# Kernel tuning notes

Measured on AMD Instinct MI355X. Metric: run time of the kernel, lower is better.

The kernel has to match this reference:

```python
import jax, jax.numpy as jnp
import numpy as np

KS = 5          # kernel_size
D = 2           # spatial dim
DX = 0.01       # region kernel spacing
SCALE = 1.0
NX, NY = 32, 32
N = NX * NY


def _region_kernel():
    # gaussians.region_kernel: KS x KS grid of offsets spaced DX, centered at 0
    off = (jnp.arange(KS, dtype=jnp.float32) - (KS - 1) / 2.0) * DX
    gx, gy = jnp.meshgrid(off, off, indexing='ij')
    return jnp.stack([gx, gy], -1).reshape(-1, D)  # (KS*KS, 2)


def _build_cov(scaling, transform):
    # Cholesky-style parameterization: L lower-triangular with diag=scaling,
    # off-diag=transform; cov = L @ L^T (d=2 closed form)
    s0, s1 = scaling[:, 0], scaling[:, 1]
    t = transform[:, 0]
    c00 = s0 * s0
    c01 = s0 * t
    c11 = t * t + s1 * s1
    return jnp.stack([jnp.stack([c00, c01], -1), jnp.stack([c01, c11], -1)], -2)


def _inv2x2(c):
    det = c[:, 0, 0] * c[:, 1, 1] - c[:, 0, 1] * c[:, 1, 0]
    inv = jnp.stack([jnp.stack([c[:, 1, 1], -c[:, 0, 1]], -1),
                     jnp.stack([-c[:, 1, 0], c[:, 0, 0]], -1)], -2)
    return inv / det[:, None, None]


def setup_inputs() -> dict:
    key = jax.random.key(0)
    ks = jax.random.split(key, 20)
    # Gaussian state: grid means as in __init__
    tx = jnp.linspace(-1.0, 1.0, NX) * SCALE
    ty = jnp.linspace(-1.0, 1.0, NY) * SCALE
    gx, gy = jnp.meshgrid(tx, ty, indexing='ij')
    means = jnp.stack([gx, gy], -1).reshape(-1, D).astype(jnp.float32)
    u = 0.1 * jax.random.normal(ks[0], (N, 1), jnp.float32)
    scaling = jnp.exp(-4.5 + 0.2 * jax.random.normal(ks[1], (N, D), jnp.float32)) * SCALE
    transform = 0.002 * jax.random.normal(ks[2], (N, 1), jnp.float32)
    opacities = 2.0 + 0.1 * jax.random.normal(ks[3], (N,), jnp.float32)
    # network weights (4 heads share the first 3 layer shapes)
    convW = 0.05 * jax.random.normal(ks[4], (4, 50, 3, KS, KS), jnp.float32)
    convb = 0.01 * jax.random.normal(ks[5], (4, 50), jnp.float32)
    embW = 0.3 * jax.random.normal(ks[6], (4, 7, 30), jnp.float32)
    embb = 0.01 * jax.random.normal(ks[7], (4, 30), jnp.float32)
    l1W = 0.1 * jax.random.normal(ks[8], (4, 80, 80), jnp.float32)
    l1b = 0.01 * jax.random.normal(ks[9], (4, 80), jnp.float32)
    outW_sol = 0.1 * jax.random.normal(ks[10], (80, 1), jnp.float32)
    outb_sol = 0.01 * jax.random.normal(ks[11], (1,), jnp.float32)
    outW_trans = 0.1 * jax.random.normal(ks[12], (80, 2), jnp.float32)
    outb_trans = 0.01 * jax.random.normal(ks[13], (2,), jnp.float32)
    outW_scale = 0.1 * jax.random.normal(ks[14], (80, 2), jnp.float32)
    outb_scale = 0.01 * jax.random.normal(ks[15], (2,), jnp.float32)
    outW_tform = 0.1 * jax.random.normal(ks[16], (80, 1), jnp.float32)
    outb_tform = 0.01 * jax.random.normal(ks[17], (1,), jnp.float32)
    return {"means": means, "u": u, "scaling": scaling, "transform": transform,
            "opacities": opacities, "convW": convW, "convb": convb,
            "embW": embW, "embb": embb, "l1W": l1W, "l1b": l1b,
            "outW_sol": outW_sol, "outb_sol": outb_sol,
            "outW_trans": outW_trans, "outb_trans": outb_trans,
            "outW_scale": outW_scale, "outb_scale": outb_scale,
            "outW_tform": outW_tform, "outb_tform": outb_tform}


def reference(means, u, scaling, transform, opacities, convW, convb, embW, embb,
              l1W, l1b, outW_sol, outb_sol, outW_trans, outb_trans,
              outW_scale, outb_scale, outW_tform, outb_tform):
    n = means.shape[0]
    cov = _build_cov(scaling, transform)          # (N,2,2)
    conics = _inv2x2(cov)                         # (N,2,2)

    # --- sampling (torch.no_grad block in original) ---
    kern = _region_kernel()                                        # (25,2)
    samples = (means[:, None, :] + kern[None]).reshape(-1, D)      # (M,2), M=N*25
    bc = jnp.all(jnp.abs(samples) < SCALE, -1).astype(means.dtype)[:, None]
    alpha = jax.nn.sigmoid(opacities)                              # (N,)
    diff = samples[:, None, :] - means[None, :, :]                 # (M,N,2)
    Cq = jnp.einsum('nij,mnj->mni', conics, diff)                  # (M,N,2)
    G = jnp.exp(-0.5 * jnp.einsum('mni,mni->mn', diff, Cq)) * alpha[None, :]  # (M,N)
    u_s = G @ u                                                    # (M,1)
    # DIFFUSION pde_rhs = trace of laplacian: sum_n G * (|C q|^2 - tr(C)) * u_n
    trC = conics[:, 0, 0] + conics[:, 1, 1]
    lap = jnp.einsum('mn,mn,nc->mc', G, (Cq ** 2).sum(-1) - trC[None, :], u)  # (M,1)
    in_samples = jax.lax.stop_gradient(jnp.concatenate([u_s, lap, bc], -1))   # (M,3)

    # (N, 25, 3) -> (N, 3, 5, 5)
    img = in_samples.reshape(n, KS * KS, -1).transpose(0, 2, 1).reshape(n, -1, KS, KS)
    in_params = jnp.concatenate([means, u, scaling, transform, opacities[:, None]], -1)  # (N,7)

    # 4 Networks: conv(5x5 -> 1x1, 50ch) + param embed(7->30) + MLP(80->80->out)
    y = jnp.tanh(jnp.einsum('ncij,kocij->kno', img, convW) + convb[:, None, :])   # (4,N,50)
    e = jnp.tanh(jnp.einsum('nf,kfg->kng', in_params, embW) + embb[:, None, :])   # (4,N,30)
    h = jnp.tanh(jnp.einsum('knf,kfg->kng', jnp.concatenate([y, e], -1), l1W)
                 + l1b[:, None, :])                                               # (4,N,80)

    deltas = h[0] @ outW_sol + outb_sol          # (N,1)
    translation = h[1] @ outW_trans + outb_trans # (N,2)
    dscale = h[2] @ outW_scale + outb_scale      # (N,2)
    dtransform = h[3] @ outW_tform + outb_tform  # (N,1)

    u_new = u + deltas
    means_new = means + translation
    scaling_new = scaling * jnp.exp(dscale)
    transform_new = transform + dtransform
    cov_new = _build_cov(scaling_new, transform_new)
    return (u_new, means_new, scaling_new, transform_new, cov_new)
```

## Files before the change

kernel.cpp:

```cpp
#include <hip/hip_runtime.h>
#include <hip/hip_bf16.h>


#define NG 1024

__device__ __forceinline__ float tanh_fast(float x) {
    return 1.0f - 2.0f / (__expf(2.0f * x) + 1.0f);
}

__global__ __launch_bounds__(256) void k_fused(
    const float* __restrict__ means, const float* __restrict__ u,
    const float* __restrict__ scal, const float* __restrict__ trans,
    const float* __restrict__ opac,
    const float* __restrict__ convW, const float* __restrict__ convb,
    const float* __restrict__ embW,  const float* __restrict__ embb,
    const float* __restrict__ l1W,   const float* __restrict__ l1b,
    const float* __restrict__ oWs,  const float* __restrict__ obs,
    const float* __restrict__ oWt,  const float* __restrict__ obt,
    const float* __restrict__ oWsc, const float* __restrict__ obsc,
    const float* __restrict__ oWtf, const float* __restrict__ obtf,
    float* __restrict__ out)
{
    __shared__ float gcomp[NG * 8];
    __shared__ float pus[2][2][32];
    __shared__ float plap[2][2][32];
    __shared__ float simg[2][80];
    __shared__ float hin[2][4][80];
    __shared__ float hv[2][4][80];
    __shared__ float semb[840];
    __shared__ float sembb[120];
    __shared__ float shead[480];
    __shared__ float sheadb[6];
    __shared__ int   cnt;

    const int t  = threadIdx.x;
    const int n0 = blockIdx.x * 2;

    const float mx0 = means[2*n0],   my0 = means[2*n0+1];
    const float mx1 = means[2*n0+2], my1 = means[2*n0+3];
    const float uu0 = u[n0],     uu1 = u[n0+1];
    const float sc00 = scal[2*n0],   sc01 = scal[2*n0+1];
    const float sc10 = scal[2*n0+2], sc11 = scal[2*n0+3];
    const float tr0 = trans[n0], tr1 = trans[n0+1];
    const float op0 = opac[n0],  op1 = opac[n0+1];

    float wcv[75];
    {
        const float* w = convW + (size_t)(t < 200 ? t : 0) * 75;
        #pragma unroll
        for (int j = 0; j < 75; ++j) wcv[j] = w[j];
    }
    float w1[80];
    {
        int k = t / 80, g = t - (t / 80) * 80;
        const float* w = l1W + (size_t)(k * 80) * 80 + g;
        #pragma unroll
        for (int f = 0; f < 80; ++f) w1[f] = w[f * 80];
    }
    float bcv  = (t < 200) ? convb[t] : 0.0f;
    float b1   = l1b[t];
    float b1k3 = l1b[256 + (t & 63)];

    for (int i = t; i < 840; i += 256) semb[i] = embW[i];
    if (t < 120) sembb[t] = embb[t];
    for (int i = t; i < 480; i += 256) {
        float v = (i < 80) ? oWs[i] : (i < 240) ? oWt[i - 80]
                : (i < 400) ? oWsc[i - 240] : oWtf[i - 400];
        shead[i] = v;
    }
    if (t < 6) sheadb[t] = (t == 0) ? obs[0] : (t < 3) ? obt[t-1]
                         : (t < 5) ? obsc[t-3] : obtf[0];

    const float bxmin = fminf(mx0, mx1) - 0.02f, bxmax = fmaxf(mx0, mx1) + 0.02f;
    const float bymin = fminf(my0, my1) - 0.02f, bymax = fmaxf(my0, my1) + 0.02f;

    if (t == 0) cnt = 0;
    __syncthreads();
    for (int g = t; g < NG; g += 256) {
        float gmx = means[2*g], gmy = means[2*g+1];
        float s0  = scal[2*g],  s1  = scal[2*g+1];
        float tt  = trans[g];
        float c00 = s0*s0, c01 = s0*tt, c11 = tt*tt + s1*s1;
        float r2  = 100.0f * (c00 + c11);
        float ddx = fmaxf(fmaxf(bxmin - gmx, gmx - bxmax), 0.0f);
        float ddy = fmaxf(fmaxf(bymin - gmy, gmy - bymax), 0.0f);
        if (ddx*ddx + ddy*ddy <= r2) {
            float idet = 1.0f / (c00*c11 - c01*c01);
            float A = c11*idet, B = -c01*idet, C = c00*idet;
            float alpha = 1.0f / (1.0f + __expf(-opac[g]));
            int slot = atomicAdd(&cnt, 1);
            float4* dst = (float4*)(gcomp + slot*8);
            dst[0] = make_float4(gmx, gmy, A, B);
            dst[1] = make_float4(C, A + C, alpha * u[g], 0.0f);
        }
    }
    __syncthreads();
    const int nsurv = cnt;

    {
        int w = t >> 6, lane = t & 63;
        int l = w >> 1;
        int hc = ((w & 1) << 1) | (lane >> 5);
        int s  = lane & 31; if (s > 24) s = 24;
        int si = s / 5, sj = s - si * 5;
        float gx = l ? mx1 : mx0, gy = l ? my1 : my0;
        float sx = gx + (float)(si - 2) * 0.01f;
        float sy = gy + (float)(sj - 2) * 0.01f;
        float us = 0.0f, lp = 0.0f;
        #pragma unroll 2
        for (int i = hc; i < nsurv; i += 4) {
            float4 a = *(const float4*)(gcomp + i*8);
            float4 b = *(const float4*)(gcomp + i*8 + 4);
            float dx = sx - a.x, dy = sy - a.y;
            float Cq0 = a.z*dx + a.w*dy;
            float Cq1 = a.w*dx + b.x*dy;
            float q   = dx*Cq0 + dy*Cq1;
            float e   = __expf(-0.5f*q) * b.z;
            us += e;
            lp += e * (Cq0*Cq0 + Cq1*Cq1 - b.y);
        }
        us += __shfl_down(us, 32);
        lp += __shfl_down(lp, 32);
        if ((lane & 31) == s && lane < 32) {
            pus[l][w & 1][s] = us; plap[l][w & 1][s] = lp;
        }
    }
    __syncthreads();

    if (t < 50) {
        int l = t / 25, s = t - l * 25;
        float us = pus[l][0][s] + pus[l][1][s];
        float lp = plap[l][0][s] + plap[l][1][s];
        int si = s / 5, sj = s - si * 5;
        float gx = l ? mx1 : mx0, gy = l ? my1 : my0;
        float sx = gx + (float)(si - 2) * 0.01f;
        float sy = gy + (float)(sj - 2) * 0.01f;
        simg[l][s]      = us;
        simg[l][25 + s] = lp;
        simg[l][50 + s] = (fabsf(sx) < 1.0f && fabsf(sy) < 1.0f) ? 1.0f : 0.0f;
    }
    __syncthreads();

    if (t < 200) {
        float a0 = bcv, a1 = bcv;
        #pragma unroll
        for (int j = 0; j < 75; ++j) {
            a0 += simg[0][j] * wcv[j];
            a1 += simg[1][j] * wcv[j];
        }
        int k = t / 50, o = t - k * 50;
        hin[0][k][o] = tanh_fast(a0);
        hin[1][k][o] = tanh_fast(a1);
    } else {
        for (int idx = t - 200; idx < 240; idx += 56) {
            int l = idx / 120, rem = idx - l * 120;
            int k = rem / 30, g = rem - k * 30;
            float acc = sembb[k * 30 + g];
            #pragma unroll
            for (int f = 0; f < 7; ++f) {
                float in0, in1;
                switch (f) {
                    case 0: in0 = mx0;  in1 = mx1;  break;
                    case 1: in0 = my0;  in1 = my1;  break;
                    case 2: in0 = uu0;  in1 = uu1;  break;
                    case 3: in0 = sc00; in1 = sc10; break;
                    case 4: in0 = sc01; in1 = sc11; break;
                    case 5: in0 = tr0;  in1 = tr1;  break;
                    default: in0 = op0; in1 = op1;  break;
                }
                acc += (l ? in1 : in0) * semb[(k*7 + f)*30 + g];
            }
            hin[l][k][50 + g] = tanh_fast(acc);
        }
    }
    __syncthreads();

    {
        int k = t / 80, g = t - (t / 80) * 80;
        float a0 = b1, a1 = b1;
        #pragma unroll
        for (int f = 0; f < 80; ++f) {
            a0 += hin[0][k][f] * w1[f];
            a1 += hin[1][k][f] * w1[f];
        }
        hv[0][k][g] = tanh_fast(a0);
        hv[1][k][g] = tanh_fast(a1);
    }
    if (t < 64) {
        int g = 16 + t;
        float a0 = b1k3, a1 = b1k3;
        #pragma unroll 8
        for (int f = 0; f < 80; ++f) {
            float w = l1W[(3*80 + f)*80 + g];
            a0 += hin[0][3][f] * w;
            a1 += hin[1][3][f] * w;
        }
        hv[0][3][g] = tanh_fast(a0);
        hv[1][3][g] = tanh_fast(a1);
    }
    __syncthreads();

    if (t < 64) {
        int l = (t / 6) & 1, t6 = t % 6;
        int k, base, stride, j;
        if (t6 == 0)      { k = 0; base = 0;   stride = 1; j = 0; }
        else if (t6 < 3)  { k = 1; base = 80;  stride = 2; j = t6 - 1; }
        else if (t6 < 5)  { k = 2; base = 240; stride = 2; j = t6 - 3; }
        else              { k = 3; base = 400; stride = 1; j = 0; }
        float acc = sheadb[t6];
        #pragma unroll 8
        for (int f = 0; f < 80; ++f)
            acc += hv[l][k][f] * shead[base + f * stride + j];

        int sb = (t / 6) * 6;
        float o0 = __shfl(acc, sb + 0);
        float o1 = __shfl(acc, sb + 1);
        float o2 = __shfl(acc, sb + 2);
        float o3 = __shfl(acc, sb + 3);
        float o4 = __shfl(acc, sb + 4);
        float o5 = __shfl(acc, sb + 5);

        if (t == 0 || t == 6) {
            int n = n0 + (t / 6);
            float uu = t ? uu1 : uu0;
            float s0 = t ? sc10 : sc00, s1 = t ? sc11 : sc01;
            float tr = t ? tr1 : tr0;
            float u_new = uu + o0;
            float mxn = (t ? mx1 : mx0) + o1;
            float myn = (t ? my1 : my0) + o2;
            float s0n = s0 * __expf(o3);
            float s1n = s1 * __expf(o4);
            float tn  = tr + o5;
            float c00 = s0n*s0n, c01 = s0n*tn, c11 = tn*tn + s1n*s1n;
            out[n]              = u_new;
            out[1024 + 2*n]     = mxn;
            out[1024 + 2*n + 1] = myn;
            out[3072 + 2*n]     = s0n;
            out[3072 + 2*n + 1] = s1n;
            out[5120 + n]       = tn;
            out[6144 + 4*n]     = c00;
            out[6144 + 4*n + 1] = c01;
            out[6144 + 4*n + 2] = c01;
            out[6144 + 4*n + 3] = c11;
        }
    }
}

extern "C" void kernel_launch(void* const* d_in, const int* in_sizes, int n_in,
                              void* d_out, int out_size, void* d_ws, size_t ws_size,
                              hipStream_t stream)
{
    k_fused<<<dim3(NG / 2), dim3(256), 0, stream>>>(
        (const float*)d_in[0],  (const float*)d_in[1],  (const float*)d_in[2],
        (const float*)d_in[3],  (const float*)d_in[4],  (const float*)d_in[5],
        (const float*)d_in[6],  (const float*)d_in[7],  (const float*)d_in[8],
        (const float*)d_in[9],  (const float*)d_in[10], (const float*)d_in[11],
        (const float*)d_in[12], (const float*)d_in[13], (const float*)d_in[14],
        (const float*)d_in[15], (const float*)d_in[16], (const float*)d_in[17],
        (const float*)d_in[18], (float*)d_out);
}
```

Baseline: 105.0 us.

## Move conv and layer-1 weights out of registers and cap the survivor buffer

Result: slower. 108.5 us (+3.4%).

```diff
diff --git a/kernel.cpp b/kernel.cpp
--- a/kernel.cpp
+++ b/kernel.cpp
@@ -3,12 +3,13 @@
 
 
 #define NG 1024
+#define GCAP 160
 
 __device__ __forceinline__ float tanh_fast(float x) {
     return 1.0f - 2.0f / (__expf(2.0f * x) + 1.0f);
 }
 
-__global__ __launch_bounds__(256) void k_fused(
+__global__ __launch_bounds__(256, 2) void k_fused(
     const float* __restrict__ means, const float* __restrict__ u,
     const float* __restrict__ scal, const float* __restrict__ trans,
     const float* __restrict__ opac,
@@ -21,7 +22,8 @@
     const float* __restrict__ oWtf, const float* __restrict__ obtf,
     float* __restrict__ out)
 {
-    __shared__ float gcomp[NG * 8];
+    __shared__ float scv[15000];
+    __shared__ float gcomp[GCAP * 8];
     __shared__ float pus[2][2][32];
     __shared__ float plap[2][2][32];
     __shared__ float simg[2][80];
@@ -44,23 +46,7 @@
     const float tr0 = trans[n0], tr1 = trans[n0+1];
     const float op0 = opac[n0],  op1 = opac[n0+1];
 
-    float wcv[75];
-    {
-        const float* w = convW + (size_t)(t < 200 ? t : 0) * 75;
-        #pragma unroll
-        for (int j = 0; j < 75; ++j) wcv[j] = w[j];
-    }
-    float w1[80];
-    {
-        int k = t / 80, g = t - (t / 80) * 80;
-        const float* w = l1W + (size_t)(k * 80) * 80 + g;
-        #pragma unroll
-        for (int f = 0; f < 80; ++f) w1[f] = w[f * 80];
-    }
-    float bcv  = (t < 200) ? convb[t] : 0.0f;
-    float b1   = l1b[t];
-    float b1k3 = l1b[256 + (t & 63)];
-
+    for (int i = t; i < 15000; i += 256) scv[i] = convW[i];
     for (int i = t; i < 840; i += 256) semb[i] = embW[i];
     if (t < 120) sembb[t] = embb[t];
     for (int i = t; i < 480; i += 256) {
@@ -89,13 +75,15 @@
             float A = c11*idet, B = -c01*idet, C = c00*idet;
             float alpha = 1.0f / (1.0f + __expf(-opac[g]));
             int slot = atomicAdd(&cnt, 1);
-            float4* dst = (float4*)(gcomp + slot*8);
-            dst[0] = make_float4(gmx, gmy, A, B);
-            dst[1] = make_float4(C, A + C, alpha * u[g], 0.0f);
-        }
-    }
-    __syncthreads();
-    const int nsurv = cnt;
+            if (slot < GCAP) {
+                float4* dst = (float4*)(gcomp + slot*8);
+                dst[0] = make_float4(gmx, gmy, A, B);
+                dst[1] = make_float4(C, A + C, alpha * u[g], 0.0f);
+            }
+        }
+    }
+    __syncthreads();
+    const int nsurv = min(cnt, GCAP);
 
     {
         int w = t >> 6, lane = t & 63;
@@ -142,11 +130,13 @@
     __syncthreads();
 
     if (t < 200) {
-        float a0 = bcv, a1 = bcv;
-        #pragma unroll
+        const float* w = scv + t * 75;
+        float a0 = convb[t], a1 = a0;
+        #pragma unroll 5
         for (int j = 0; j < 75; ++j) {
-            a0 += simg[0][j] * wcv[j];
-            a1 += simg[1][j] * wcv[j];
+            float wj = w[j];
+            a0 += simg[0][j] * wj;
+            a1 += simg[1][j] * wj;
         }
         int k = t / 50, o = t - k * 50;
         hin[0][k][o] = tanh_fast(a0);
@@ -177,21 +167,22 @@
 
     {
         int k = t / 80, g = t - (t / 80) * 80;
-        float a0 = b1, a1 = b1;
-        #pragma unroll
+        float a0 = l1b[t], a1 = a0;
+        #pragma unroll 8
         for (int f = 0; f < 80; ++f) {
-            a0 += hin[0][k][f] * w1[f];
-            a1 += hin[1][k][f] * w1[f];
+            float w = l1W[(k*80 + f)*80 + g];
+            a0 += hin[0][k][f] * w;
+            a1 += hin[1][k][f] * w;
         }
         hv[0][k][g] = tanh_fast(a0);
         hv[1][k][g] = tanh_fast(a1);
     }
     if (t < 64) {
         int g = 16 + t;
-        float a0 = b1k3, a1 = b1k3;
+        float a0 = l1b[256 + t], a1 = a0;
         #pragma unroll 8
         for (int f = 0; f < 80; ++f) {
-            float w = l1W[(3*80 + f)*80 + g];
+            float w = l1W[(240 + f)*80 + g];
             a0 += hin[0][3][f] * w;
             a1 += hin[1][3][f] * w;
         }
```
